# Optimization experiments

Hardware: AMD Instinct MI355X
Metric: run time of the kernel (lower is better)

The kernel has to match this reference:

```python
import jax, jax.numpy as jnp
import numpy as np

N = 50000
E = 800000
FEAT = 512
HID = 256
CLS = 40
EPS = 1e-5


def setup_inputs() -> dict:
    key = jax.random.key(0)
    ks = jax.random.split(key, 8)
    x = jax.random.normal(ks[0], (N, FEAT), dtype=jnp.float32)
    edge_index = jax.random.randint(ks[1], (2, E), 0, N, dtype=jnp.int64)
    s = 0.05
    return {
        "x": x,
        "edge_index": edge_index,
        "W1": jax.random.normal(ks[2], (FEAT, HID), dtype=jnp.float32) * s,
        "b1": jnp.zeros((HID,), jnp.float32),
        "W2": jax.random.normal(ks[3], (HID, HID), dtype=jnp.float32) * s,
        "b2": jnp.zeros((HID,), jnp.float32),
        "W3": jax.random.normal(ks[4], (HID, CLS), dtype=jnp.float32) * s,
        "b3": jnp.zeros((CLS,), jnp.float32),
        "gamma": jnp.ones((HID,), jnp.float32),
        "beta": jnp.zeros((HID,), jnp.float32),
        "run_mean": jnp.zeros((HID,), jnp.float32),
        "run_var": jnp.ones((HID,), jnp.float32),
    }


def _edge_norm(edge_index):
    # add self-loops, then symmetric normalization D^-1/2 (A+I) D^-1/2
    loop = jnp.arange(N, dtype=edge_index.dtype)
    src = jnp.concatenate([edge_index[0], loop])
    dst = jnp.concatenate([edge_index[1], loop])
    deg = jax.ops.segment_sum(jnp.ones_like(dst, jnp.float32), dst, num_segments=N)
    inv_sqrt = jnp.where(deg > 0, jax.lax.rsqrt(jnp.maximum(deg, 1.0)), 0.0)
    norm = inv_sqrt[src] * inv_sqrt[dst]  # [E+N]
    return src, dst, norm


def _gcn_conv(x, W, b, src, dst, norm):
    h = x @ W                               # [N, out]
    msg = h[src] * norm[:, None]            # gather + scale, [E+N, out]
    out = jax.ops.segment_sum(msg, dst, num_segments=N)
    return out + b


def _bn_relu(x, gamma, beta, mean, var):
    return jax.nn.relu((x - mean) * jax.lax.rsqrt(var + EPS) * gamma + beta)


def reference(x, edge_index, W1, b1, W2, b2, W3, b3, gamma, beta, run_mean, run_var):
    src, dst, norm = _edge_norm(edge_index)
    h = _gcn_conv(x, W1, b1, src, dst, norm)
    h = _bn_relu(h, gamma, beta, run_mean, run_var)
    h = _gcn_conv(h, W2, b2, src, dst, norm)
    h = _bn_relu(h, gamma, beta, run_mean, run_var)
    h = _gcn_conv(h, W3, b3, src, dst, norm)
    return h
```

## Files before the change

kernel.cpp:

```cpp
#include <hip/hip_runtime.h>
#include <cstdint>
#include <cstddef>

#define FEAT 512
#define HID 256
#define CLS 40
#define EPS 1e-5f

typedef __attribute__((ext_vector_type(8))) short short8;
typedef __attribute__((ext_vector_type(4))) float f32x4v;


__device__ __forceinline__ unsigned short f2bf(float f) {
    union { float f; unsigned u; } v; v.f = f;
    unsigned r = v.u + 0x7FFF + ((v.u >> 16) & 1);
    return (unsigned short)(r >> 16);
}
__device__ __forceinline__ float bf2f(unsigned short h) {
    union { unsigned u; float f; } v; v.u = ((unsigned)h) << 16;
    return v.f;
}

typedef const __attribute__((address_space(1))) unsigned int* gas_ptr;
typedef __attribute__((address_space(3))) unsigned int* las_ptr;
__device__ __forceinline__ void lds_load16(const void* g, void* l) {
    __builtin_amdgcn_global_load_lds((gas_ptr)g, (las_ptr)l, 16, 0, 0);
}

__device__ __forceinline__ float4 f4add(float4 a, float4 b) {
    return make_float4(a.x + b.x, a.y + b.y, a.z + b.z, a.w + b.w);
}

__device__ __forceinline__ void accum_bf4(float4& a, ushort4 v) {
    a.x += bf2f(v.x); a.y += bf2f(v.y); a.z += bf2f(v.z); a.w += bf2f(v.w);
}


__global__ __launch_bounds__(256) void prep_cvt_kernel(
        const float* __restrict__ x, const float* __restrict__ W1, const float* __restrict__ W2,
        int* __restrict__ counts, int* __restrict__ fillpos,
        unsigned short* __restrict__ w1hi, unsigned short* __restrict__ w1lo,
        unsigned short* __restrict__ w2hi, unsigned short* __restrict__ w2lo,
        unsigned short* __restrict__ xbf, int N) {
    int i = blockIdx.x * 256 + threadIdx.x;
    const int n0 = N;
    const int n1 = FEAT * HID;
    const int n2 = HID * HID;
    const int n3 = N * FEAT / 8;
    if (i < n0) { counts[i] = 0; fillpos[i] = 0; return; }
    i -= n0;
    if (i < n1) {
        int k = i / HID, n = i % HID;
        float f = W1[i];
        unsigned short h = f2bf(f);
        w1hi[(size_t)n * FEAT + k] = h;
        w1lo[(size_t)n * FEAT + k] = f2bf(f - bf2f(h));
        return;
    }
    i -= n1;
    if (i < n2) {
        int k = i / HID, n = i % HID;
        float f = W2[i];
        unsigned short h = f2bf(f);
        w2hi[(size_t)n * HID + k] = h;
        w2lo[(size_t)n * HID + k] = f2bf(f - bf2f(h));
        return;
    }
    i -= n2;
    if (i < n3) {
        const float4* xp = (const float4*)x;
        float4 a = xp[2 * i], b = xp[2 * i + 1];
        float f[8] = {a.x, a.y, a.z, a.w, b.x, b.y, b.z, b.w};
        short8 h;
#pragma unroll
        for (int j = 0; j < 8; ++j) h[j] = (short)f2bf(f[j]);
        ((short8*)xbf)[i] = h;
    }
}


__global__ void hist_kernel(const int* __restrict__ dst, int* __restrict__ counts, int E) {
    int e = blockIdx.x * 256 + threadIdx.x;
    if (e < E) atomicAdd(&counts[dst[e]], 1);
}

__global__ void scan_block_kernel(const int* __restrict__ counts, int* __restrict__ row_ptr,
                                  int* __restrict__ blocksums, int n) {
    __shared__ int s[256];
    int tid = threadIdx.x;
    int i = blockIdx.x * 256 + tid;
    int v = (i < n) ? counts[i] : 0;
    s[tid] = v; __syncthreads();
    for (int off = 1; off < 256; off <<= 1) {
        int t = (tid >= off) ? s[tid - off] : 0;
        __syncthreads();
        s[tid] += t;
        __syncthreads();
    }
    if (i < n) row_ptr[i] = s[tid] - v;
    if (tid == 255) blocksums[blockIdx.x] = s[255];
}

__global__ void finalize_rowptr_kernel(int* __restrict__ row_ptr, const int* __restrict__ blocksums,
                                       const int* __restrict__ counts, float* __restrict__ inv_sqrt,
                                       int n, int E, int nb) {
    __shared__ int s[256];
    __shared__ int excl[256];
    int tid = threadIdx.x;
    int v = (tid < nb) ? blocksums[tid] : 0;
    s[tid] = v; __syncthreads();
    for (int off = 1; off < 256; off <<= 1) {
        int t = (tid >= off) ? s[tid - off] : 0;
        __syncthreads();
        s[tid] += t;
        __syncthreads();
    }
    excl[tid] = s[tid] - v;
    __syncthreads();
    int i = blockIdx.x * 256 + tid;
    if (i < n) {
        row_ptr[i] += excl[i >> 8];
        inv_sqrt[i] = rsqrtf((float)(counts[i] + 1));
    }
    if (i == 0) row_ptr[n] = E;
}

__global__ void fill_kernel(const int* __restrict__ src, const int* __restrict__ dst,
                            const int* __restrict__ row_ptr, int* __restrict__ fillpos,
                            int* __restrict__ src_sorted, int E) {
    int e = blockIdx.x * 256 + threadIdx.x;
    if (e < E) {
        int d = dst[e];
        int pos = row_ptr[d] + atomicAdd(&fillpos[d], 1);
        src_sorted[pos] = src[e];
    }
}


template<int K>
__global__ __launch_bounds__(512) void gemm_mfma_pipe_kernel(
        const unsigned short* __restrict__ gA,
        const unsigned short* __restrict__ Wthi, const unsigned short* __restrict__ Wtlo,
        const float* __restrict__ inv_sqrt, unsigned short* __restrict__ C,
        int M) {
    constexpr int NT = K / 32;
    __shared__ unsigned short Abuf [3][16 * 512];
    __shared__ unsigned short Bhbuf[3][16 * 512];
    __shared__ unsigned short Blbuf[3][16 * 512];
    const int tid  = threadIdx.x;
    const int lane = tid & 63;
    const int w    = tid >> 6;
    const int wr   = w >> 2, wc = w & 3;
    const int lm   = lane & 15;
    const int lk8  = (lane >> 4) * 8;
    const int bm   = blockIdx.x * 256;

    f32x4v acc[8][4] = {};

    int ar0 = bm + 16 * w + lm;       if (ar0 >= M) ar0 = M - 1;
    int ar1 = bm + 128 + 16 * w + lm; if (ar1 >= M) ar1 = M - 1;
    const unsigned short* gA0  = gA   + (size_t)ar0 * K + lk8;
    const unsigned short* gA1  = gA   + (size_t)ar1 * K + lk8;
    const unsigned short* gBh0 = Wthi + (size_t)(16 * (2 * w)     + lm) * K + lk8;
    const unsigned short* gBh1 = Wthi + (size_t)(16 * (2 * w + 1) + lm) * K + lk8;
    const unsigned short* gBl0 = Wtlo + (size_t)(16 * (2 * w)     + lm) * K + lk8;
    const unsigned short* gBl1 = Wtlo + (size_t)(16 * (2 * w + 1) + lm) * K + lk8;

    auto stage = [&](int buf, int t) {
        const int kg = t * 32;
        lds_load16(gA0  + kg, &Abuf [buf][w * 512]);
        lds_load16(gA1  + kg, &Abuf [buf][(8 + w) * 512]);
        lds_load16(gBh0 + kg, &Bhbuf[buf][(2 * w) * 512]);
        lds_load16(gBh1 + kg, &Bhbuf[buf][(2 * w + 1) * 512]);
        lds_load16(gBl0 + kg, &Blbuf[buf][(2 * w) * 512]);
        lds_load16(gBl1 + kg, &Blbuf[buf][(2 * w + 1) * 512]);
    };

    auto compute = [&](int buf) {
        short8 ah[8], bh[4], bv[4];
#pragma unroll
        for (int j = 0; j < 4; ++j) {
            bh[j] = *(const short8*)&Bhbuf[buf][(wc * 4 + j) * 512 + lane * 8];
            bv[j] = *(const short8*)&Blbuf[buf][(wc * 4 + j) * 512 + lane * 8];
        }
#pragma unroll
        for (int i = 0; i < 8; ++i)
            ah[i] = *(const short8*)&Abuf[buf][(wr * 8 + i) * 512 + lane * 8];
#pragma unroll
        for (int i = 0; i < 8; ++i)
#pragma unroll
            for (int j = 0; j < 4; ++j) {
                acc[i][j] = __builtin_amdgcn_mfma_f32_16x16x32_bf16(ah[i], bh[j], acc[i][j], 0, 0, 0);
                acc[i][j] = __builtin_amdgcn_mfma_f32_16x16x32_bf16(ah[i], bv[j], acc[i][j], 0, 0, 0);
            }
    };

    stage(0, 0); stage(1, 1); stage(2, 2);
    asm volatile("s_waitcnt vmcnt(12)" ::: "memory");
    __builtin_amdgcn_s_barrier();
    __builtin_amdgcn_sched_barrier(0);

#pragma unroll
    for (int t = 0; t < NT; ++t) {
        const int buf = t % 3;
        compute(buf);
        __builtin_amdgcn_s_barrier();
        __builtin_amdgcn_sched_barrier(0);
        if (t + 3 < NT) {
            stage(buf, t + 3);
            asm volatile("s_waitcnt vmcnt(12)" ::: "memory");
        } else if (t + 2 < NT) {
            asm volatile("s_waitcnt vmcnt(6)" ::: "memory");
        } else if (t + 1 < NT) {
            asm volatile("s_waitcnt vmcnt(0)" ::: "memory");
        }
        __builtin_amdgcn_s_barrier();
        __builtin_amdgcn_sched_barrier(0);
    }

    const int orow_base = bm + wr * 128;
    const int ocol_base = wc * 64 + lm;
    const int rq = (lane >> 4) * 4;
#pragma unroll
    for (int i = 0; i < 8; ++i) {
#pragma unroll
        for (int r = 0; r < 4; ++r) {
            int row = orow_base + i * 16 + rq + r;
            if (row >= M) continue;
            float s = inv_sqrt[row];
            size_t rb = (size_t)row * HID;
#pragma unroll
            for (int j = 0; j < 4; ++j)
                C[rb + ocol_base + j * 16] = f2bf(acc[i][j][r] * s);
        }
    }
}


__global__ __launch_bounds__(256) void gemm_scaled_hl_kernel(
        const unsigned short* __restrict__ Ahi, const unsigned short* __restrict__ Alo,
        const float* __restrict__ W,
        const float* __restrict__ inv_sqrt, float* __restrict__ C,
        int M, int K, int Ncol) {
    __shared__ float As[16][64];
    __shared__ float Ws[16][64];
    int tid = threadIdx.x;
    int tm = tid >> 4;
    int tn = tid & 15;
    int bm = blockIdx.x * 64;
    int bn = blockIdx.y * 64;

    float acc[4][4] = {};

    int lr = tid >> 2;
    int lc = (tid & 3) << 2;
    int wr = tid >> 4;
    int wc = (tid & 15) << 2;
    int arow = bm + lr;
    bool aok = arow < M;
    bool wok = (bn + wc) < Ncol;
    const unsigned short* AhiRow = Ahi + (size_t)arow * K + lc;
    const unsigned short* AloRow = Alo + (size_t)arow * K + lc;

    for (int k0 = 0; k0 < K; k0 += 16) {
        float4 av = make_float4(0.f, 0.f, 0.f, 0.f);
        if (aok) {
            ushort4 hv = *(const ushort4*)(AhiRow + k0);
            ushort4 lv = *(const ushort4*)(AloRow + k0);
            av.x = bf2f(hv.x) + bf2f(lv.x);
            av.y = bf2f(hv.y) + bf2f(lv.y);
            av.z = bf2f(hv.z) + bf2f(lv.z);
            av.w = bf2f(hv.w) + bf2f(lv.w);
        }
        As[lc + 0][lr] = av.x; As[lc + 1][lr] = av.y;
        As[lc + 2][lr] = av.z; As[lc + 3][lr] = av.w;

        float4 wv = make_float4(0.f, 0.f, 0.f, 0.f);
        if (wok) wv = *(const float4*)(W + (size_t)(k0 + wr) * Ncol + bn + wc);
        *(float4*)&Ws[wr][wc] = wv;
        __syncthreads();

#pragma unroll
        for (int k = 0; k < 16; ++k) {
            const float4 a4 = *(const float4*)&As[k][tm << 2];
            const float4 b4 = *(const float4*)&Ws[k][tn << 2];
            float a[4] = {a4.x, a4.y, a4.z, a4.w};
            float b[4] = {b4.x, b4.y, b4.z, b4.w};
#pragma unroll
            for (int i = 0; i < 4; ++i)
#pragma unroll
                for (int j = 0; j < 4; ++j)
                    acc[i][j] = fmaf(a[i], b[j], acc[i][j]);
        }
        __syncthreads();
    }

#pragma unroll
    for (int i = 0; i < 4; ++i) {
        int row = bm + (tm << 2) + i;
        if (row >= M) continue;
        float s = inv_sqrt[row];
        int col = bn + (tn << 2);
        if (col < Ncol) {
            float4 o = make_float4(acc[i][0] * s, acc[i][1] * s, acc[i][2] * s, acc[i][3] * s);
            *(float4*)&C[(size_t)row * Ncol + col] = o;
        }
    }
}


template<bool WRITE_LO>
__global__ __launch_bounds__(256) void agg_bn_hl_kernel(
        const unsigned short* __restrict__ g, const int* __restrict__ row_ptr,
        const int* __restrict__ srcs, const float* __restrict__ inv_sqrt,
        const float* __restrict__ bias, const float* __restrict__ gamma,
        const float* __restrict__ beta, const float* __restrict__ mean,
        const float* __restrict__ var,
        unsigned short* __restrict__ out_hi, unsigned short* __restrict__ out_lo, int n) {
    int node = (blockIdx.x << 2) + (threadIdx.x >> 6);
    int lane = threadIdx.x & 63;
    if (node >= n) return;
    const ushort4* gp = (const ushort4*)g;
    float4 acc0 = make_float4(0.f, 0.f, 0.f, 0.f);
    float4 acc1 = make_float4(0.f, 0.f, 0.f, 0.f);
    accum_bf4(acc0, gp[(size_t)node * 64 + lane]);
    int beg = row_ptr[node];
    int cnt = row_ptr[node + 1] - beg;

    for (int base = 0; base < cnt; base += 64) {
        int m = cnt - base; if (m > 64) m = 64;
        int idx = (lane < m) ? srcs[beg + base + lane] : 0;
        int j = 0;
        for (; j + 8 <= m; j += 8) {
            int s0 = __shfl(idx, j + 0), s1 = __shfl(idx, j + 1);
            int s2 = __shfl(idx, j + 2), s3 = __shfl(idx, j + 3);
            int s4 = __shfl(idx, j + 4), s5 = __shfl(idx, j + 5);
            int s6 = __shfl(idx, j + 6), s7 = __shfl(idx, j + 7);
            ushort4 v0 = gp[(size_t)s0 * 64 + lane];
            ushort4 v1 = gp[(size_t)s1 * 64 + lane];
            ushort4 v2 = gp[(size_t)s2 * 64 + lane];
            ushort4 v3 = gp[(size_t)s3 * 64 + lane];
            ushort4 v4 = gp[(size_t)s4 * 64 + lane];
            ushort4 v5 = gp[(size_t)s5 * 64 + lane];
            ushort4 v6 = gp[(size_t)s6 * 64 + lane];
            ushort4 v7 = gp[(size_t)s7 * 64 + lane];
            accum_bf4(acc0, v0); accum_bf4(acc0, v1);
            accum_bf4(acc0, v2); accum_bf4(acc0, v3);
            accum_bf4(acc1, v4); accum_bf4(acc1, v5);
            accum_bf4(acc1, v6); accum_bf4(acc1, v7);
        }
        for (; j < m; ++j) {
            int s = __shfl(idx, j);
            accum_bf4(acc0, gp[(size_t)s * 64 + lane]);
        }
    }
    float4 acc = f4add(acc0, acc1);

    float inv = inv_sqrt[node];
    float4 b4  = ((const float4*)bias)[lane];
    float4 ga4 = ((const float4*)gamma)[lane];
    float4 be4 = ((const float4*)beta)[lane];
    float4 m4  = ((const float4*)mean)[lane];
    float4 v4  = ((const float4*)var)[lane];
    float4 o;
    o.x = fmaxf((acc.x * inv + b4.x - m4.x) * (ga4.x * rsqrtf(v4.x + EPS)) + be4.x, 0.f);
    o.y = fmaxf((acc.y * inv + b4.y - m4.y) * (ga4.y * rsqrtf(v4.y + EPS)) + be4.y, 0.f);
    o.z = fmaxf((acc.z * inv + b4.z - m4.z) * (ga4.z * rsqrtf(v4.z + EPS)) + be4.z, 0.f);
    o.w = fmaxf((acc.w * inv + b4.w - m4.w) * (ga4.w * rsqrtf(v4.w + EPS)) + be4.w, 0.f);
    ushort4 oh;
    oh.x = f2bf(o.x); oh.y = f2bf(o.y); oh.z = f2bf(o.z); oh.w = f2bf(o.w);
    ((ushort4*)out_hi)[(size_t)node * 64 + lane] = oh;
    if (WRITE_LO) {
        ushort4 ol;
        ol.x = f2bf(o.x - bf2f(oh.x));
        ol.y = f2bf(o.y - bf2f(oh.y));
        ol.z = f2bf(o.z - bf2f(oh.z));
        ol.w = f2bf(o.w - bf2f(oh.w));
        ((ushort4*)out_lo)[(size_t)node * 64 + lane] = ol;
    }
}


__global__ __launch_bounds__(256) void agg_final_kernel(
        const float* __restrict__ g, const int* __restrict__ row_ptr,
        const int* __restrict__ srcs, const float* __restrict__ inv_sqrt,
        const float* __restrict__ bias, float* __restrict__ out, int n) {
    int node = (blockIdx.x << 2) + (threadIdx.x >> 6);
    int lane = threadIdx.x & 63;
    if (node >= n) return;
    int flane = (lane < CLS) ? lane : 0;
    float acc0 = g[(size_t)node * CLS + flane];
    float acc1 = 0.f;
    int beg = row_ptr[node];
    int cnt = row_ptr[node + 1] - beg;

    for (int base = 0; base < cnt; base += 64) {
        int m = cnt - base; if (m > 64) m = 64;
        int idx = (lane < m) ? srcs[beg + base + lane] : 0;
        int j = 0;
        for (; j + 8 <= m; j += 8) {
            int s0 = __shfl(idx, j + 0), s1 = __shfl(idx, j + 1);
            int s2 = __shfl(idx, j + 2), s3 = __shfl(idx, j + 3);
            int s4 = __shfl(idx, j + 4), s5 = __shfl(idx, j + 5);
            int s6 = __shfl(idx, j + 6), s7 = __shfl(idx, j + 7);
            float v0 = g[(size_t)s0 * CLS + flane];
            float v1 = g[(size_t)s1 * CLS + flane];
            float v2 = g[(size_t)s2 * CLS + flane];
            float v3 = g[(size_t)s3 * CLS + flane];
            float v4 = g[(size_t)s4 * CLS + flane];
            float v5 = g[(size_t)s5 * CLS + flane];
            float v6 = g[(size_t)s6 * CLS + flane];
            float v7 = g[(size_t)s7 * CLS + flane];
            acc0 += (v0 + v1) + (v2 + v3);
            acc1 += (v4 + v5) + (v6 + v7);
        }
        for (; j < m; ++j) {
            int s = __shfl(idx, j);
            acc0 += g[(size_t)s * CLS + flane];
        }
    }
    if (lane < CLS)
        out[(size_t)node * CLS + lane] = (acc0 + acc1) * inv_sqrt[node] + bias[lane];
}


extern "C" void kernel_launch(void* const* d_in, const int* in_sizes, int n_in,
                              void* d_out, int out_size, void* d_ws, size_t ws_size,
                              hipStream_t stream) {
    const float* x     = (const float*)d_in[0];
    const int*   edges = (const int*)d_in[1];
    const float* W1    = (const float*)d_in[2];
    const float* b1    = (const float*)d_in[3];
    const float* W2    = (const float*)d_in[4];
    const float* b2    = (const float*)d_in[5];
    const float* W3    = (const float*)d_in[6];
    const float* b3    = (const float*)d_in[7];
    const float* gamma = (const float*)d_in[8];
    const float* beta  = (const float*)d_in[9];
    const float* mean  = (const float*)d_in[10];
    const float* var   = (const float*)d_in[11];

    const int N = in_sizes[0] / FEAT;
    const int E = in_sizes[1] / 2;
    const int* src = edges;
    const int* dst = edges + E;

    char* ws = (char*)d_ws;
    auto alloc = [&](size_t bytes) -> char* {
        char* p = ws;
        ws += (bytes + 255) & ~(size_t)255;
        return p;
    };
    int*   counts     = (int*)  alloc((size_t)N * 4);
    int*   fillpos    = (int*)  alloc((size_t)N * 4);
    int*   row_ptr    = (int*)  alloc((size_t)(N + 1) * 4);
    int*   blocksums  = (int*)  alloc(256 * 4);
    float* inv_sqrt   = (float*)alloc((size_t)N * 4);
    int*   src_sorted = (int*)  alloc((size_t)E * 4);
    unsigned short* w1hi = (unsigned short*)alloc((size_t)FEAT * HID * 2);
    unsigned short* w1lo = (unsigned short*)alloc((size_t)FEAT * HID * 2);
    unsigned short* w2hi = (unsigned short*)alloc((size_t)HID * HID * 2);
    unsigned short* w2lo = (unsigned short*)alloc((size_t)HID * HID * 2);
    unsigned short* g    = (unsigned short*)alloc((size_t)N * HID * 2);
    unsigned short* h_hi = (unsigned short*)alloc((size_t)N * HID * 2);
    unsigned short* h_lo = (unsigned short*)alloc((size_t)N * HID * 2);
    unsigned short* xbf  = h_hi;

    int nb = (N + 255) / 256;
    int eb = (E + 255) / 256;

    int prep_items = N + FEAT * HID + HID * HID + N * FEAT / 8;
    prep_cvt_kernel<<<(prep_items + 255) / 256, 256, 0, stream>>>(
        x, W1, W2, counts, fillpos, w1hi, w1lo, w2hi, w2lo, xbf, N);
    hist_kernel<<<eb, 256, 0, stream>>>(dst, counts, E);
    scan_block_kernel<<<nb, 256, 0, stream>>>(counts, row_ptr, blocksums, N);
    finalize_rowptr_kernel<<<nb, 256, 0, stream>>>(row_ptr, blocksums, counts, inv_sqrt, N, E, nb);
    fill_kernel<<<eb, 256, 0, stream>>>(src, dst, row_ptr, fillpos, src_sorted, E);

    dim3 pipe_grid((N + 255) / 256);
    dim3 gemm3_grid((N + 63) / 64, 1);
    dim3 agg_grid((N + 3) / 4);

    gemm_mfma_pipe_kernel<FEAT><<<pipe_grid, 512, 0, stream>>>(
        xbf, w1hi, w1lo, inv_sqrt, g, N);
    agg_bn_hl_kernel<false><<<agg_grid, 256, 0, stream>>>(g, row_ptr, src_sorted, inv_sqrt,
                                                          b1, gamma, beta, mean, var, h_hi, nullptr, N);
    gemm_mfma_pipe_kernel<HID><<<pipe_grid, 512, 0, stream>>>(
        h_hi, w2hi, w2lo, inv_sqrt, g, N);
    agg_bn_hl_kernel<true><<<agg_grid, 256, 0, stream>>>(g, row_ptr, src_sorted, inv_sqrt,
                                                         b2, gamma, beta, mean, var, h_hi, h_lo, N);
    float* g3 = (float*)g;
    gemm_scaled_hl_kernel<<<gemm3_grid, 256, 0, stream>>>(h_hi, h_lo, W3, inv_sqrt, g3, N, HID, CLS);
    agg_final_kernel<<<agg_grid, 256, 0, stream>>>(g3, row_ptr, src_sorted, inv_sqrt,
                                                   b3, (float*)d_out, N);
}
```

Measured before the change: 519.0 us.

## Switch activations to K-tiled 32-column panel layout and tile aggregation by feature slice

All bf16 activation and weight buffers now use a panel layout of 32 contiguous features per row, with panels stacked along K, and the GEMMs, conversion and epilogues index it accordingly. The hidden-layer aggregation kernels launch a second grid dimension over 8 feature panels. Each wave handles one node and one 32-feature slice, with 8 lanes per neighbor and 8 neighbors gathered at once, then combines them with a cross-lane shuffle reduction. The aim is to shrink the per-pass gather working set so each panel of the 50000x256 table stays in cache, and to make GEMM tile loads contiguous. The cost is reading indices 8 times, extra shuffles, and only one eighth of lanes doing useful stores.

```diff
diff --git a/kernel.cpp b/kernel.cpp
--- a/kernel.cpp
+++ b/kernel.cpp
@@ -34,6 +34,7 @@
 __device__ __forceinline__ void accum_bf4(float4& a, ushort4 v) {
     a.x += bf2f(v.x); a.y += bf2f(v.y); a.z += bf2f(v.z); a.w += bf2f(v.w);
 }
+
 
 
 __global__ __launch_bounds__(256) void prep_cvt_kernel(
@@ -50,31 +51,36 @@
     if (i < n0) { counts[i] = 0; fillpos[i] = 0; return; }
     i -= n0;
     if (i < n1) {
-        int k = i / HID, n = i % HID;
+        int k = i / HID, nn = i % HID;
         float f = W1[i];
         unsigned short h = f2bf(f);
-        w1hi[(size_t)n * FEAT + k] = h;
-        w1lo[(size_t)n * FEAT + k] = f2bf(f - bf2f(h));
+        size_t t = ((size_t)(k >> 5) * HID + nn) * 32 + (k & 31);
+        w1hi[t] = h;
+        w1lo[t] = f2bf(f - bf2f(h));
         return;
     }
     i -= n1;
     if (i < n2) {
-        int k = i / HID, n = i % HID;
+        int k = i / HID, nn = i % HID;
         float f = W2[i];
         unsigned short h = f2bf(f);
-        w2hi[(size_t)n * HID + k] = h;
-        w2lo[(size_t)n * HID + k] = f2bf(f - bf2f(h));
+        size_t t = ((size_t)(k >> 5) * HID + nn) * 32 + (k & 31);
+        w2hi[t] = h;
+        w2lo[t] = f2bf(f - bf2f(h));
         return;
     }
     i -= n2;
     if (i < n3) {
+        int r  = i >> 6;
+        int f0 = (i & 63) << 3;
         const float4* xp = (const float4*)x;
         float4 a = xp[2 * i], b = xp[2 * i + 1];
         float f[8] = {a.x, a.y, a.z, a.w, b.x, b.y, b.z, b.w};
         short8 h;
 #pragma unroll
         for (int j = 0; j < 8; ++j) h[j] = (short)f2bf(f[j]);
-        ((short8*)xbf)[i] = h;
+        size_t t = ((size_t)(f0 >> 5) * N + r) * 32 + (f0 & 31);
+        *(short8*)(xbf + t) = h;
     }
 }
 
@@ -159,21 +165,24 @@
 
     int ar0 = bm + 16 * w + lm;       if (ar0 >= M) ar0 = M - 1;
     int ar1 = bm + 128 + 16 * w + lm; if (ar1 >= M) ar1 = M - 1;
-    const unsigned short* gA0  = gA   + (size_t)ar0 * K + lk8;
-    const unsigned short* gA1  = gA   + (size_t)ar1 * K + lk8;
-    const unsigned short* gBh0 = Wthi + (size_t)(16 * (2 * w)     + lm) * K + lk8;
-    const unsigned short* gBh1 = Wthi + (size_t)(16 * (2 * w + 1) + lm) * K + lk8;
-    const unsigned short* gBl0 = Wtlo + (size_t)(16 * (2 * w)     + lm) * K + lk8;
-    const unsigned short* gBl1 = Wtlo + (size_t)(16 * (2 * w + 1) + lm) * K + lk8;
+    const size_t tsA = (size_t)M * 32;
+    const size_t tsB = (size_t)HID * 32;
+    const unsigned short* gA0  = gA   + (size_t)ar0 * 32 + lk8;
+    const unsigned short* gA1  = gA   + (size_t)ar1 * 32 + lk8;
+    const unsigned short* gBh0 = Wthi + (size_t)(16 * (2 * w)     + lm) * 32 + lk8;
+    const unsigned short* gBh1 = Wthi + (size_t)(16 * (2 * w + 1) + lm) * 32 + lk8;
+    const unsigned short* gBl0 = Wtlo + (size_t)(16 * (2 * w)     + lm) * 32 + lk8;
+    const unsigned short* gBl1 = Wtlo + (size_t)(16 * (2 * w + 1) + lm) * 32 + lk8;
 
     auto stage = [&](int buf, int t) {
-        const int kg = t * 32;
-        lds_load16(gA0  + kg, &Abuf [buf][w * 512]);
-        lds_load16(gA1  + kg, &Abuf [buf][(8 + w) * 512]);
-        lds_load16(gBh0 + kg, &Bhbuf[buf][(2 * w) * 512]);
-        lds_load16(gBh1 + kg, &Bhbuf[buf][(2 * w + 1) * 512]);
-        lds_load16(gBl0 + kg, &Blbuf[buf][(2 * w) * 512]);
-        lds_load16(gBl1 + kg, &Blbuf[buf][(2 * w + 1) * 512]);
+        const size_t oA = (size_t)t * tsA;
+        const size_t oB = (size_t)t * tsB;
+        lds_load16(gA0  + oA, &Abuf [buf][w * 512]);
+        lds_load16(gA1  + oA, &Abuf [buf][(8 + w) * 512]);
+        lds_load16(gBh0 + oB, &Bhbuf[buf][(2 * w) * 512]);
+        lds_load16(gBh1 + oB, &Bhbuf[buf][(2 * w + 1) * 512]);
+        lds_load16(gBl0 + oB, &Blbuf[buf][(2 * w) * 512]);
+        lds_load16(gBl1 + oB, &Blbuf[buf][(2 * w + 1) * 512]);
     };
 
     auto compute = [&](int buf) {
@@ -219,7 +228,6 @@
     }
 
     const int orow_base = bm + wr * 128;
-    const int ocol_base = wc * 64 + lm;
     const int rq = (lane >> 4) * 4;
 #pragma unroll
     for (int i = 0; i < 8; ++i) {
@@ -228,10 +236,11 @@
             int row = orow_base + i * 16 + rq + r;
             if (row >= M) continue;
             float s = inv_sqrt[row];
-            size_t rb = (size_t)row * HID;
-#pragma unroll
-            for (int j = 0; j < 4; ++j)
-                C[rb + ocol_base + j * 16] = f2bf(acc[i][j][r] * s);
+#pragma unroll
+            for (int j = 0; j < 4; ++j) {
+                size_t off = ((size_t)(wc * 2 + (j >> 1)) * M + row) * 32 + lm + (j & 1) * 16;
+                C[off] = f2bf(acc[i][j][r] * s);
+            }
         }
     }
 }
@@ -259,14 +268,13 @@
     int arow = bm + lr;
     bool aok = arow < M;
     bool wok = (bn + wc) < Ncol;
-    const unsigned short* AhiRow = Ahi + (size_t)arow * K + lc;
-    const unsigned short* AloRow = Alo + (size_t)arow * K + lc;
 
     for (int k0 = 0; k0 < K; k0 += 16) {
         float4 av = make_float4(0.f, 0.f, 0.f, 0.f);
         if (aok) {
-            ushort4 hv = *(const ushort4*)(AhiRow + k0);
-            ushort4 lv = *(const ushort4*)(AloRow + k0);
+            size_t ta = ((size_t)(k0 >> 5) * M + arow) * 32 + (k0 & 16) + lc;
+            ushort4 hv = *(const ushort4*)(Ahi + ta);
+            ushort4 lv = *(const ushort4*)(Alo + ta);
             av.x = bf2f(hv.x) + bf2f(lv.x);
             av.y = bf2f(hv.y) + bf2f(lv.y);
             av.z = bf2f(hv.z) + bf2f(lv.z);
@@ -310,73 +318,83 @@
 
 
 template<bool WRITE_LO>
-__global__ __launch_bounds__(256) void agg_bn_hl_kernel(
+__global__ __launch_bounds__(256) void agg_bn_tiled_kernel(
         const unsigned short* __restrict__ g, const int* __restrict__ row_ptr,
         const int* __restrict__ srcs, const float* __restrict__ inv_sqrt,
         const float* __restrict__ bias, const float* __restrict__ gamma,
         const float* __restrict__ beta, const float* __restrict__ mean,
         const float* __restrict__ var,
         unsigned short* __restrict__ out_hi, unsigned short* __restrict__ out_lo, int n) {
-    int node = (blockIdx.x << 2) + (threadIdx.x >> 6);
-    int lane = threadIdx.x & 63;
+    __shared__ int sidx[4][64];
+    const int wv   = threadIdx.x >> 6;
+    const int lane = threadIdx.x & 63;
+    const int node = (blockIdx.x << 2) + wv;
+    const int p    = blockIdx.y;
     if (node >= n) return;
-    const ushort4* gp = (const ushort4*)g;
-    float4 acc0 = make_float4(0.f, 0.f, 0.f, 0.f);
-    float4 acc1 = make_float4(0.f, 0.f, 0.f, 0.f);
-    accum_bf4(acc0, gp[(size_t)node * 64 + lane]);
+    const int gi = lane >> 3;
+    const int ci = lane & 7;
+    const ushort4* gp = (const ushort4*)(g + (size_t)p * n * 32);
+
+    float4 a0 = {0.f,0.f,0.f,0.f}, a1 = {0.f,0.f,0.f,0.f};
+
+    if (gi == 0) {
+        ushort4 v = gp[(size_t)node * 8 + ci];
+        accum_bf4(a0, v);
+    }
     int beg = row_ptr[node];
     int cnt = row_ptr[node + 1] - beg;
 
     for (int base = 0; base < cnt; base += 64) {
         int m = cnt - base; if (m > 64) m = 64;
-        int idx = (lane < m) ? srcs[beg + base + lane] : 0;
+        sidx[wv][lane] = (lane < m) ? srcs[beg + base + lane] : 0;
         int j = 0;
-        for (; j + 8 <= m; j += 8) {
-            int s0 = __shfl(idx, j + 0), s1 = __shfl(idx, j + 1);
-            int s2 = __shfl(idx, j + 2), s3 = __shfl(idx, j + 3);
-            int s4 = __shfl(idx, j + 4), s5 = __shfl(idx, j + 5);
-            int s6 = __shfl(idx, j + 6), s7 = __shfl(idx, j + 7);
-            ushort4 v0 = gp[(size_t)s0 * 64 + lane];
-            ushort4 v1 = gp[(size_t)s1 * 64 + lane];
-            ushort4 v2 = gp[(size_t)s2 * 64 + lane];
-            ushort4 v3 = gp[(size_t)s3 * 64 + lane];
-            ushort4 v4 = gp[(size_t)s4 * 64 + lane];
-            ushort4 v5 = gp[(size_t)s5 * 64 + lane];
-            ushort4 v6 = gp[(size_t)s6 * 64 + lane];
-            ushort4 v7 = gp[(size_t)s7 * 64 + lane];
-            accum_bf4(acc0, v0); accum_bf4(acc0, v1);
-            accum_bf4(acc0, v2); accum_bf4(acc0, v3);
-            accum_bf4(acc1, v4); accum_bf4(acc1, v5);
-            accum_bf4(acc1, v6); accum_bf4(acc1, v7);
-        }
-        for (; j < m; ++j) {
-            int s = __shfl(idx, j);
-            accum_bf4(acc0, gp[(size_t)s * 64 + lane]);
-        }
-    }
-    float4 acc = f4add(acc0, acc1);
+        for (; j + 16 <= m; j += 16) {
+            int s0 = sidx[wv][j + gi];
+            int s1 = sidx[wv][j + 8 + gi];
+            ushort4 v0 = gp[(size_t)s0 * 8 + ci];
+            ushort4 v1 = gp[(size_t)s1 * 8 + ci];
+            accum_bf4(a0, v0);
+            accum_bf4(a1, v1);
+        }
+        for (; j < m; j += 8) {
+            int jj = j + gi;
+            int s = sidx[wv][jj < m ? jj : j];
+            ushort4 v = gp[(size_t)s * 8 + ci];
+            if (jj < m) accum_bf4(a0, v);
+        }
+    }
+    float4 acc = f4add(a0, a1);
+#pragma unroll
+    for (int off = 8; off < 64; off <<= 1) {
+        acc.x += __shfl_xor(acc.x, off);
+        acc.y += __shfl_xor(acc.y, off);
+        acc.z += __shfl_xor(acc.z, off);
+        acc.w += __shfl_xor(acc.w, off);
+    }
 
     float inv = inv_sqrt[node];
-    float4 b4  = ((const float4*)bias)[lane];
-    float4 ga4 = ((const float4*)gamma)[lane];
-    float4 be4 = ((const float4*)beta)[lane];
-    float4 m4  = ((const float4*)mean)[lane];
-    float4 v4  = ((const float4*)var)[lane];
+    int fb = p * 8 + ci;
+    float4 b4 = ((const float4*)bias)[fb];
+    float4 ga = ((const float4*)gamma)[fb];
+    float4 be = ((const float4*)beta)[fb];
+    float4 mu = ((const float4*)mean)[fb];
+    float4 vr = ((const float4*)var)[fb];
     float4 o;
-    o.x = fmaxf((acc.x * inv + b4.x - m4.x) * (ga4.x * rsqrtf(v4.x + EPS)) + be4.x, 0.f);
-    o.y = fmaxf((acc.y * inv + b4.y - m4.y) * (ga4.y * rsqrtf(v4.y + EPS)) + be4.y, 0.f);
-    o.z = fmaxf((acc.z * inv + b4.z - m4.z) * (ga4.z * rsqrtf(v4.z + EPS)) + be4.z, 0.f);
-    o.w = fmaxf((acc.w * inv + b4.w - m4.w) * (ga4.w * rsqrtf(v4.w + EPS)) + be4.w, 0.f);
+    o.x = fmaxf((acc.x * inv + b4.x - mu.x) * (ga.x * rsqrtf(vr.x + EPS)) + be.x, 0.f);
+    o.y = fmaxf((acc.y * inv + b4.y - mu.y) * (ga.y * rsqrtf(vr.y + EPS)) + be.y, 0.f);
+    o.z = fmaxf((acc.z * inv + b4.z - mu.z) * (ga.z * rsqrtf(vr.z + EPS)) + be.z, 0.f);
+    o.w = fmaxf((acc.w * inv + b4.w - mu.w) * (ga.w * rsqrtf(vr.w + EPS)) + be.w, 0.f);
     ushort4 oh;
     oh.x = f2bf(o.x); oh.y = f2bf(o.y); oh.z = f2bf(o.z); oh.w = f2bf(o.w);
-    ((ushort4*)out_hi)[(size_t)node * 64 + lane] = oh;
-    if (WRITE_LO) {
+    size_t widx = (size_t)p * n * 8 + (size_t)node * 8 + ci;
+    if (gi == 0) ((ushort4*)out_hi)[widx] = oh;
+    if (WRITE_LO && gi == 1) {
         ushort4 ol;
         ol.x = f2bf(o.x - bf2f(oh.x));
         ol.y = f2bf(o.y - bf2f(oh.y));
         ol.z = f2bf(o.z - bf2f(oh.z));
         ol.w = f2bf(o.w - bf2f(oh.w));
-        ((ushort4*)out_lo)[(size_t)node * 64 + lane] = ol;
+        ((ushort4*)out_lo)[widx] = ol;
     }
 }
 
@@ -479,16 +497,17 @@
 
     dim3 pipe_grid((N + 255) / 256);
     dim3 gemm3_grid((N + 63) / 64, 1);
+    dim3 aggt_grid((N + 3) / 4, 8);
     dim3 agg_grid((N + 3) / 4);
 
     gemm_mfma_pipe_kernel<FEAT><<<pipe_grid, 512, 0, stream>>>(
         xbf, w1hi, w1lo, inv_sqrt, g, N);
-    agg_bn_hl_kernel<false><<<agg_grid, 256, 0, stream>>>(g, row_ptr, src_sorted, inv_sqrt,
-                                                          b1, gamma, beta, mean, var, h_hi, nullptr, N);
+    agg_bn_tiled_kernel<false><<<aggt_grid, 256, 0, stream>>>(g, row_ptr, src_sorted, inv_sqrt,
+                                                              b1, gamma, beta, mean, var, h_hi, nullptr, N);
     gemm_mfma_pipe_kernel<HID><<<pipe_grid, 512, 0, stream>>>(
         h_hi, w2hi, w2lo, inv_sqrt, g, N);
-    agg_bn_hl_kernel<true><<<agg_grid, 256, 0, stream>>>(g, row_ptr, src_sorted, inv_sqrt,
-                                                         b2, gamma, beta, mean, var, h_hi, h_lo, N);
+    agg_bn_tiled_kernel<true><<<aggt_grid, 256, 0, stream>>>(g, row_ptr, src_sorted, inv_sqrt,
+                                                             b2, gamma, beta, mean, var, h_hi, h_lo, N);
     float* g3 = (float*)g;
     gemm_scaled_hl_kernel<<<gemm3_grid, 256, 0, stream>>>(h_hi, h_lo, W3, inv_sqrt, g3, N, HID, CLS);
     agg_final_kernel<<<agg_grid, 256, 0, stream>>>(g3, row_ptr, src_sorted, inv_sqrt,
```

After: 708.8 us. 1.37x slower.
